# Kernel optimization log

Hardware: AMD Instinct MI355X
Metric: run time of the kernel (lower is better)

The kernel has to match this reference:

```python
import jax, jax.numpy as jnp
import numpy as np
from jax import lax

FIRE_RATE = 0.5
CLIP_ALPHA = 0.1

def _sobel_kernels_3d():
    # (4,1,3,3,3): identity, grad-x, grad-y, grad-z
    g = np.array([1.0, 2.0, 1.0], np.float32)
    s = np.array([1.0, 0.0, -1.0], np.float32)
    sx = np.einsum('i,j,k->ijk', s, g, g) / 16.0
    sy = np.einsum('i,j,k->ijk', g, s, g) / 16.0
    sz = np.einsum('i,j,k->ijk', g, g, s) / 16.0
    ident = np.zeros((3, 3, 3), np.float32)
    ident[1, 1, 1] = 1.0
    return jnp.asarray(np.stack([ident, sx, sy, sz])[:, None])

_KERN = _sobel_kernels_3d()

def _life_mask(state):
    # alive if 3x3x3 max-pooled alpha channel > CLIP_ALPHA
    alpha = state[:, 3:4]
    pooled = lax.reduce_window(alpha, -jnp.inf, lax.max,
                               (1, 1, 3, 3, 3), (1, 1, 1, 1, 1), 'SAME')
    return (pooled > CLIP_ALPHA).astype(state.dtype)

def _perceive(state):
    # depthwise application of the 4 fixed kernels, replicate padding
    n, c, d, h, w = state.shape
    padded = jnp.pad(state, ((0, 0), (0, 0), (1, 1), (1, 1), (1, 1)), mode='edge')
    x = padded.reshape(n * c, 1, d + 2, h + 2, w + 2)
    y = lax.conv_general_dilated(x, _KERN.astype(state.dtype), (1, 1, 1), 'VALID',
                                 dimension_numbers=('NCDHW', 'OIDHW', 'NCDHW'))
    # (n*c,4,d,h,w) -> (n,4,c,d,h,w) -> (n,4c,d,h,w) matches torch concat order
    y = y.reshape(n, c, 4, d, h, w).transpose(0, 2, 1, 3, 4, 5)
    return y.reshape(n, 4 * c, d, h, w)

def setup_inputs() -> dict:
    key = jax.random.key(0)
    k1, k2, k3, k4 = jax.random.split(key, 4)
    N, C, G, H = 4, 16, 64, 96
    state = jax.random.normal(k1, (N, C, G, G, G), dtype=jnp.float32)
    rand_u = jax.random.uniform(k2, (N, 1, G, G, G), dtype=jnp.float32)
    w1 = jax.random.normal(k3, (H, 4 * C), dtype=jnp.float32) * 0.05
    b1 = jnp.zeros((H,), jnp.float32)
    w2 = jax.random.normal(k4, (C, H), dtype=jnp.float32) * 0.05
    return {"state": state, "rand_u": rand_u, "w1": w1, "b1": b1, "w2": w2}

def reference(state, rand_u, w1, b1, w2):
    pre_alive = _life_mask(state)
    perception = _perceive(state)                       # (N,4C,D,H,W)
    hid = jnp.einsum('nxdhw,yx->nydhw', perception, w1) + b1[None, :, None, None, None]
    hid = jax.nn.relu(hid)
    delta = jnp.einsum('nydhw,cy->ncdhw', hid, w2)      # (N,C,D,H,W)
    update_mask = (rand_u < FIRE_RATE).astype(state.dtype)
    new_state = state + delta * update_mask
    post_alive = _life_mask(new_state)
    return new_state * (pre_alive * post_alive)
```

## Files before the change

### kernel.cpp

```cpp
#include <hip/hip_runtime.h>

constexpr int G = 64;
constexpr int C = 16;
constexpr int NBATCH = 4;
constexpr int HID = 96;
constexpr int G3 = G * G * G;

typedef _Float16 h2    __attribute__((ext_vector_type(2)));
typedef _Float16 f16x4 __attribute__((ext_vector_type(4)));
typedef _Float16 f16x8 __attribute__((ext_vector_type(8)));
typedef float    f32x4 __attribute__((ext_vector_type(4)));

__device__ __forceinline__ f32x4 mfma16(f16x8 a, f16x8 b, f32x4 c) {
    return __builtin_amdgcn_mfma_f32_16x16x32_f16(a, b, c, 0, 0, 0);
}

#if __has_builtin(__builtin_amdgcn_global_load_lds)
#define HAS_GLL 1
__device__ __forceinline__ void gload_lds(const float* g, float* l) {
    __builtin_amdgcn_global_load_lds(
        (const __attribute__((address_space(1))) void*)g,
        (__attribute__((address_space(3))) void*)l, 4, 0, 0);
}
#else
#define HAS_GLL 0
#endif

__global__ __launch_bounds__(256)
void nca_packw(const float* __restrict__ w1, const float* __restrict__ w2,
               _Float16* __restrict__ a1p, _Float16* __restrict__ a2p)
{
    const int i = blockIdx.x * 256 + threadIdx.x;
    {
        const int j = i & 7, lane = (i >> 3) & 63, f = i >> 9;
        const int mt = f >> 1, kt = f & 1;
        const int y = mt * 16 + (lane & 15);
        const int x = kt * 32 + ((lane >> 4) << 3) + j;
        a1p[i] = (_Float16)w1[y * 64 + x];
    }
    if (i < 3 * 512) {
        const int j = i & 7, lane = (i >> 3) & 63, kt2 = i >> 9;
        const int c = lane & 15;
        const int y = kt2 * 32 + ((lane >> 4) << 3) + j;
        a2p[i] = (_Float16)w2[c * HID + y];
    }
}

constexpr int HALO_N = 600;
constexpr int BUF_F  = 8 * HALO_N;
constexpr int XROW = 144;
constexpr int HROW = 80;
constexpr int XWAVE = 64 * XROW;

__global__ __launch_bounds__(256, 3)
void nca_update(const float* __restrict__ state, const float* __restrict__ rand_u,
                const _Float16* __restrict__ a1p, const float* __restrict__ b1,
                const _Float16* __restrict__ a2p,
                float* __restrict__ out, float* __restrict__ acopy)
{
    __shared__ __align__(16) char smem[2 * BUF_F * 4];
    float* buf0 = (float*)smem;
    float* buf1 = buf0 + BUF_F;

    const int tid = threadIdx.x;
    const int bid = blockIdx.x;
    const int bx = bid & 7, by = (bid >> 3) & 7, bz = (bid >> 6) & 15, n = bid >> 10;
    const int x0 = bx * 8, y0 = by * 8, z0 = bz * 4;
    const float* sb = state + (size_t)n * C * G3;

    int vo0, vo1, vo2;
    {
        const int j = tid;
        const int lx = j % 10, t = j / 10, ly = t % 10, lz = t / 10;
        vo0 = min(max(z0 + lz - 1, 0), G - 1) * (G * G)
            + min(max(y0 + ly - 1, 0), G - 1) * G
            + min(max(x0 + lx - 1, 0), G - 1);
    }
    {
        const int j = tid + 256;
        const int lx = j % 10, t = j / 10, ly = t % 10, lz = t / 10;
        vo1 = min(max(z0 + lz - 1, 0), G - 1) * (G * G)
            + min(max(y0 + ly - 1, 0), G - 1) * G
            + min(max(x0 + lx - 1, 0), G - 1);
    }
    const bool act2 = (tid + 512 < HALO_N);
    {
        const int j = min(tid + 512, HALO_N - 1);
        const int lx = j % 10, t = j / 10, ly = t % 10, lz = t / 10;
        vo2 = min(max(z0 + lz - 1, 0), G - 1) * (G * G)
            + min(max(y0 + ly - 1, 0), G - 1) * G
            + min(max(x0 + lx - 1, 0), G - 1);
    }
    const int wbase = tid & ~63;

    const int lxl = (tid & 7) + 1, lyl = ((tid >> 3) & 7) + 1, lzl = (tid >> 6) + 1;
    const int cbase = (lzl - 1) * 100 + (lyl - 1) * 10 + (lxl - 1);
    const size_t vofs = (size_t)(z0 + lzl - 1) * (G * G)
                      + (size_t)(y0 + lyl - 1) * G + (x0 + lxl - 1);
    const float ru = rand_u[(size_t)n * G3 + vofs];

#if HAS_GLL
#pragma unroll
    for (int c = 0; c < 8; ++c) {
        const float* gc = sb + (size_t)c * G3;
        gload_lds(gc + vo0, buf0 + c * HALO_N + wbase);
        gload_lds(gc + vo1, buf0 + c * HALO_N + 256 + wbase);
        if (act2) gload_lds(gc + vo2, buf0 + c * HALO_N + 512 + wbase);
    }
    __syncthreads();

#pragma unroll
    for (int c = 0; c < 8; ++c) {
        const float* gc = sb + (size_t)(8 + c) * G3;
        gload_lds(gc + vo0, buf1 + c * HALO_N + wbase);
        gload_lds(gc + vo1, buf1 + c * HALO_N + 256 + wbase);
        if (act2) gload_lds(gc + vo2, buf1 + c * HALO_N + 512 + wbase);
    }
#else
#pragma unroll
    for (int c = 0; c < 8; ++c) {
        const float* gc = sb + (size_t)c * G3;
        buf0[c * HALO_N + tid] = gc[vo0];
        buf0[c * HALO_N + 256 + tid] = gc[vo1];
        if (act2) buf0[c * HALO_N + 512 + tid] = gc[vo2];
    }
    __syncthreads();
#pragma unroll
    for (int c = 0; c < 8; ++c) {
        const float* gc = sb + (size_t)(8 + c) * G3;
        buf1[c * HALO_N + tid] = gc[vo0];
        buf1[c * HALO_N + 256 + tid] = gc[vo1];
        if (act2) buf1[c * HALO_N + 512 + tid] = gc[vo2];
    }
#endif

    h2 pp[32];
    float ctrf[C];
    float pf0 = 0.f, pf1 = 0.f, pf2 = 0.f, pf3 = 0.f;
    float amax = -3.0e38f;

#pragma unroll
    for (int g = 0; g < 2; ++g) {
        const float* bb = g ? buf1 : buf0;
        if (g) __syncthreads();

#pragma unroll
        for (int c = 0; c < 8; ++c) {
            const int cg = g * 8 + c;
            const float* buf = bb + c * HALO_N;
            float P0 = 0.f, P2 = 0.f, U0 = 0.f, U2 = 0.f, V0 = 0.f, V2 = 0.f;
            float ctr = 0.f, mx = -3.0e38f;
#pragma unroll
            for (int dz = 0; dz < 3; ++dz) {
                const float gzw = (dz == 1) ? 2.f : 1.f;
#pragma unroll
                for (int dy = 0; dy < 3; ++dy) {
                    const float gyw = (dy == 1) ? 2.f : 1.f;
                    const float* r = buf + cbase + dz * 100 + dy * 10;
                    const float a0 = r[0], a1 = r[1], a2 = r[2];
                    const float rs = a0 + 2.f * a1 + a2;
                    if (dz == 0) P0 += gyw * rs;
                    if (dz == 2) P2 += gyw * rs;
                    if (dy == 0) U0 += gzw * rs;
                    if (dy == 2) U2 += gzw * rs;
                    V0 += gzw * gyw * a0;
                    V2 += gzw * gyw * a2;
                    if (dz == 1 && dy == 1) ctr = a1;
                    if (cg == 3) mx = fmaxf(mx, fmaxf(fmaxf(a0, a1), a2));
                }
            }
            if (cg == 3) amax = mx;
            ctrf[cg] = ctr;

            const float f0 = ctr;
            const float f1 = (P0 - P2) * 0.0625f;
            const float f2 = (U0 - U2) * 0.0625f;
            const float f3 = (V0 - V2) * 0.0625f;

            if (cg & 1) {
                const int j = cg >> 1;
                h2 v;
                v.x = (_Float16)pf0; v.y = (_Float16)f0; pp[j]      = v;
                v.x = (_Float16)pf1; v.y = (_Float16)f1; pp[8 + j]  = v;
                v.x = (_Float16)pf2; v.y = (_Float16)f2; pp[16 + j] = v;
                v.x = (_Float16)pf3; v.y = (_Float16)f3; pp[24 + j] = v;
            } else {
                pf0 = f0; pf1 = f1; pf2 = f2; pf3 = f3;
            }
        }
    }

    __syncthreads();

    const float pre = (amax > 0.1f) ? 1.f : 0.f;

    const int lane = tid & 63;
    const int w    = tid >> 6;
    const int l15  = lane & 15;
    const int lg   = lane >> 4;
    char* xw = smem + w * XWAVE;

#pragma unroll
    for (int q = 0; q < 8; ++q) {
        uint4 t;
        t.x = __builtin_bit_cast(unsigned, pp[4 * q]);
        t.y = __builtin_bit_cast(unsigned, pp[4 * q + 1]);
        t.z = __builtin_bit_cast(unsigned, pp[4 * q + 2]);
        t.w = __builtin_bit_cast(unsigned, pp[4 * q + 3]);
        *(uint4*)(xw + lane * XROW + q * 16) = t;
    }

    f16x8 bfr[8];
#pragma unroll
    for (int kt = 0; kt < 2; ++kt)
#pragma unroll
        for (int nt = 0; nt < 4; ++nt)
            bfr[kt * 4 + nt] = *(const f16x8*)(xw + (nt * 16 + l15) * XROW + kt * 64 + lg * 16);

    const f16x8* a1 = ((const f16x8*)a1p) + lane;
    const f16x8* a2 = ((const f16x8*)a2p) + lane;

    f32x4 acc2[4];
#pragma unroll
    for (int nt = 0; nt < 4; ++nt) acc2[nt] = (f32x4){0.f, 0.f, 0.f, 0.f};

#pragma unroll 1
    for (int kt2 = 0; kt2 < 3; ++kt2) {
#pragma unroll
        for (int mtsub = 0; mtsub < 2; ++mtsub) {
            const int mt = kt2 * 2 + mtsub;
            const f16x8 a_0 = a1[(mt * 2 + 0) * 64];
            const f16x8 a_1 = a1[(mt * 2 + 1) * 64];
            const f32x4 bias = *(const f32x4*)(b1 + mt * 16 + lg * 4);
#pragma unroll
            for (int nt = 0; nt < 4; ++nt) {
                f32x4 acc = (f32x4){0.f, 0.f, 0.f, 0.f};
                acc = mfma16(a_0, bfr[nt],     acc);
                acc = mfma16(a_1, bfr[4 + nt], acc);
                f16x4 hv;
                hv[0] = (_Float16)fmaxf(acc[0] + bias[0], 0.f);
                hv[1] = (_Float16)fmaxf(acc[1] + bias[1], 0.f);
                hv[2] = (_Float16)fmaxf(acc[2] + bias[2], 0.f);
                hv[3] = (_Float16)fmaxf(acc[3] + bias[3], 0.f);
                *(f16x4*)(xw + (nt * 16 + l15) * HROW + mtsub * 32 + lg * 8) = hv;
            }
        }
        const f16x8 a2f = a2[kt2 * 64];
#pragma unroll
        for (int nt = 0; nt < 4; ++nt) {
            const f16x8 b2 = *(const f16x8*)(xw + (nt * 16 + l15) * HROW + lg * 16);
            acc2[nt] = mfma16(a2f, b2, acc2[nt]);
        }
    }

#pragma unroll
    for (int nt = 0; nt < 4; ++nt) {
        *(f32x4*)(xw + (nt * 16 + l15) * HROW + lg * 16) = acc2[nt];
    }

    const float m = (ru < 0.5f) ? 1.f : 0.f;
    float* ob = out + (size_t)n * C * G3;
    float* ac = acopy + (size_t)n * G3;
#pragma unroll
    for (int q = 0; q < 4; ++q) {
        const f32x4 dv = *(const f32x4*)(xw + lane * HROW + q * 16);
#pragma unroll
        for (int r = 0; r < 4; ++r) {
            const int c = q * 4 + r;
            const float nv = fmaf(dv[r], m, ctrf[c]);
            if (c == 3) ac[vofs] = nv;
            ob[(size_t)c * G3 + vofs] = nv * pre;
        }
    }
}

__global__ __launch_bounds__(256)
void nca_post(const float* __restrict__ acopy, float* __restrict__ out)
{
    const int idx = blockIdx.x * 256 + threadIdx.x;
    const int n = idx >> 18;
    const int v = idx & (G3 - 1);
    const int x = v & 63, y = (v >> 6) & 63, z = v >> 12;
    const float* ab = acopy + (size_t)n * G3;
    float mx = -3.0e38f;
#pragma unroll
    for (int dz = -1; dz <= 1; ++dz) {
        const int zz = min(max(z + dz, 0), G - 1);
#pragma unroll
        for (int dy = -1; dy <= 1; ++dy) {
            const int yy = min(max(y + dy, 0), G - 1);
            const int xm = max(x - 1, 0), xp = min(x + 1, G - 1);
            const float* row = ab + (size_t)zz * (G * G) + (size_t)yy * G;
            mx = fmaxf(mx, fmaxf(fmaxf(row[xm], row[x]), row[xp]));
        }
    }
    if (mx > 0.1f) return;
    float* ob = out + (size_t)n * C * G3 + v;
#pragma unroll
    for (int c = 0; c < C; ++c) ob[(size_t)c * G3] = 0.f;
}

extern "C" void kernel_launch(void* const* d_in, const int* in_sizes, int n_in,
                              void* d_out, int out_size, void* d_ws, size_t ws_size,
                              hipStream_t stream)
{
    const float* state  = (const float*)d_in[0];
    const float* rand_u = (const float*)d_in[1];
    const float* w1     = (const float*)d_in[2];
    const float* b1     = (const float*)d_in[3];
    const float* w2     = (const float*)d_in[4];
    float* out  = (float*)d_out;

    _Float16* a1p  = (_Float16*)d_ws;
    _Float16* a2p  = (_Float16*)((char*)d_ws + 12 * 1024);
    float*    acop = (float*)((char*)d_ws + 16 * 1024);

    nca_packw <<<24, 256, 0, stream>>>(w1, w2, a1p, a2p);
    nca_update<<<NBATCH * 8 * 8 * 16, 256, 0, stream>>>(state, rand_u, a1p, b1, a2p, out, acop);
    nca_post  <<<(NBATCH * G3) / 256, 256, 0, stream>>>(acop, out);
}
```

Measured before the change: 111.4 us.

## Pipeline halo loads in four channel groups and raise occupancy with LDS swizzle

Halo staging now streams four groups of four channels through a ping-pong LDS buffer, so the global-to-LDS loads for the next group overlap the stencil work on the current one. The launch bound rises from 3 to 4 blocks per CU. To cut register use, the per-channel center values are no longer kept in fp32 registers; they are read back from an fp16 side buffer in LDS for the residual add. The MFMA operand tile drops its padding and uses an XOR swizzle to avoid bank conflicts. The trade-offs are more barriers per block and fp16 rounding of the state term in the output, which may affect accuracy.

```diff
diff --git a/kernel.cpp b/kernel.cpp
--- a/kernel.cpp
+++ b/kernel.cpp
@@ -47,20 +47,22 @@
 }
 
 constexpr int HALO_N = 600;
-constexpr int BUF_F  = 8 * HALO_N;
-constexpr int XROW = 144;
-constexpr int HROW = 80;
-constexpr int XWAVE = 64 * XROW;
-
-__global__ __launch_bounds__(256, 3)
+constexpr int GBUF_F = 4 * HALO_N;
+constexpr int XROW   = 128;
+constexpr int XWAVE  = 64 * XROW;
+constexpr int HROW   = 80;
+constexpr int SIDE_OFF = 4 * XWAVE;
+constexpr int SMEM_B = SIDE_OFF + 256 * 32;
+
+__global__ __launch_bounds__(256, 4)
 void nca_update(const float* __restrict__ state, const float* __restrict__ rand_u,
                 const _Float16* __restrict__ a1p, const float* __restrict__ b1,
                 const _Float16* __restrict__ a2p,
                 float* __restrict__ out, float* __restrict__ acopy)
 {
-    __shared__ __align__(16) char smem[2 * BUF_F * 4];
-    float* buf0 = (float*)smem;
-    float* buf1 = buf0 + BUF_F;
+    __shared__ __align__(16) char smem[SMEM_B];
+    float* bufA = (float*)smem;
+    float* bufB = bufA + GBUF_F;
 
     const int tid = threadIdx.x;
     const int bid = blockIdx.x;
@@ -99,54 +101,50 @@
                       + (size_t)(y0 + lyl - 1) * G + (x0 + lxl - 1);
     const float ru = rand_u[(size_t)n * G3 + vofs];
 
-#if HAS_GLL
-#pragma unroll
-    for (int c = 0; c < 8; ++c) {
-        const float* gc = sb + (size_t)c * G3;
-        gload_lds(gc + vo0, buf0 + c * HALO_N + wbase);
-        gload_lds(gc + vo1, buf0 + c * HALO_N + 256 + wbase);
-        if (act2) gload_lds(gc + vo2, buf0 + c * HALO_N + 512 + wbase);
-    }
-    __syncthreads();
-
-#pragma unroll
-    for (int c = 0; c < 8; ++c) {
-        const float* gc = sb + (size_t)(8 + c) * G3;
-        gload_lds(gc + vo0, buf1 + c * HALO_N + wbase);
-        gload_lds(gc + vo1, buf1 + c * HALO_N + 256 + wbase);
-        if (act2) gload_lds(gc + vo2, buf1 + c * HALO_N + 512 + wbase);
-    }
-#else
-#pragma unroll
-    for (int c = 0; c < 8; ++c) {
-        const float* gc = sb + (size_t)c * G3;
-        buf0[c * HALO_N + tid] = gc[vo0];
-        buf0[c * HALO_N + 256 + tid] = gc[vo1];
-        if (act2) buf0[c * HALO_N + 512 + tid] = gc[vo2];
-    }
-    __syncthreads();
-#pragma unroll
-    for (int c = 0; c < 8; ++c) {
-        const float* gc = sb + (size_t)(8 + c) * G3;
-        buf1[c * HALO_N + tid] = gc[vo0];
-        buf1[c * HALO_N + 256 + tid] = gc[vo1];
-        if (act2) buf1[c * HALO_N + 512 + tid] = gc[vo2];
-    }
-#endif
-
     h2 pp[32];
-    float ctrf[C];
     float pf0 = 0.f, pf1 = 0.f, pf2 = 0.f, pf3 = 0.f;
     float amax = -3.0e38f;
 
-#pragma unroll
-    for (int g = 0; g < 2; ++g) {
-        const float* bb = g ? buf1 : buf0;
-        if (g) __syncthreads();
-
-#pragma unroll
-        for (int c = 0; c < 8; ++c) {
-            const int cg = g * 8 + c;
+#if HAS_GLL
+#define STAGE(gi, dst)                                                       \
+    {                                                                        \
+        const float* s4 = sb + (size_t)((gi) * 4) * G3;                      \
+        _Pragma("unroll")                                                    \
+        for (int c = 0; c < 4; ++c) {                                        \
+            const float* gc = s4 + (size_t)c * G3;                           \
+            gload_lds(gc + vo0, (dst) + c * HALO_N + wbase);                 \
+            gload_lds(gc + vo1, (dst) + c * HALO_N + 256 + wbase);           \
+            if (act2) gload_lds(gc + vo2, (dst) + c * HALO_N + 512 + wbase); \
+        }                                                                    \
+    }
+#else
+#define STAGE(gi, dst)                                                       \
+    {                                                                        \
+        const float* s4 = sb + (size_t)((gi) * 4) * G3;                      \
+        _Pragma("unroll")                                                    \
+        for (int c = 0; c < 4; ++c) {                                        \
+            const float* gc = s4 + (size_t)c * G3;                           \
+            (dst)[c * HALO_N + tid] = gc[vo0];                               \
+            (dst)[c * HALO_N + 256 + tid] = gc[vo1];                         \
+            if (act2) (dst)[c * HALO_N + 512 + tid] = gc[vo2];               \
+        }                                                                    \
+    }
+#endif
+
+    STAGE(0, bufA);
+    __syncthreads();
+
+#pragma unroll
+    for (int g = 0; g < 4; ++g) {
+        if (g < 3) {
+            float* nb = (g & 1) ? bufA : bufB;
+            STAGE(g + 1, nb);
+        }
+        const float* bb = (g & 1) ? bufB : bufA;
+
+#pragma unroll
+        for (int c = 0; c < 4; ++c) {
+            const int cg = g * 4 + c;
             const float* buf = bb + c * HALO_N;
             float P0 = 0.f, P2 = 0.f, U0 = 0.f, U2 = 0.f, V0 = 0.f, V2 = 0.f;
             float ctr = 0.f, mx = -3.0e38f;
@@ -170,7 +168,6 @@
                 }
             }
             if (cg == 3) amax = mx;
-            ctrf[cg] = ctr;
 
             const float f0 = ctr;
             const float f1 = (P0 - P2) * 0.0625f;
@@ -188,9 +185,9 @@
                 pf0 = f0; pf1 = f1; pf2 = f2; pf3 = f3;
             }
         }
-    }
-
-    __syncthreads();
+        __syncthreads();
+    }
+#undef STAGE
 
     const float pre = (amax > 0.1f) ? 1.f : 0.f;
 
@@ -198,7 +195,22 @@
     const int w    = tid >> 6;
     const int l15  = lane & 15;
     const int lg   = lane >> 4;
-    char* xw = smem + w * XWAVE;
+    char* xw   = smem + w * XWAVE;
+    char* side = smem + SIDE_OFF + tid * 32;
+
+    {
+        uint4 ia, ib;
+        ia.x = __builtin_bit_cast(unsigned, pp[0]);
+        ia.y = __builtin_bit_cast(unsigned, pp[1]);
+        ia.z = __builtin_bit_cast(unsigned, pp[2]);
+        ia.w = __builtin_bit_cast(unsigned, pp[3]);
+        ib.x = __builtin_bit_cast(unsigned, pp[4]);
+        ib.y = __builtin_bit_cast(unsigned, pp[5]);
+        ib.z = __builtin_bit_cast(unsigned, pp[6]);
+        ib.w = __builtin_bit_cast(unsigned, pp[7]);
+        *(uint4*)(side) = ia;
+        *(uint4*)(side + 16) = ib;
+    }
 
 #pragma unroll
     for (int q = 0; q < 8; ++q) {
@@ -207,15 +219,18 @@
         t.y = __builtin_bit_cast(unsigned, pp[4 * q + 1]);
         t.z = __builtin_bit_cast(unsigned, pp[4 * q + 2]);
         t.w = __builtin_bit_cast(unsigned, pp[4 * q + 3]);
-        *(uint4*)(xw + lane * XROW + q * 16) = t;
+        *(uint4*)(xw + lane * XROW + ((q * 16) ^ ((lane & 7) << 4))) = t;
     }
 
     f16x8 bfr[8];
 #pragma unroll
     for (int kt = 0; kt < 2; ++kt)
 #pragma unroll
-        for (int nt = 0; nt < 4; ++nt)
-            bfr[kt * 4 + nt] = *(const f16x8*)(xw + (nt * 16 + l15) * XROW + kt * 64 + lg * 16);
+        for (int nt = 0; nt < 4; ++nt) {
+            const int v = nt * 16 + l15;
+            bfr[kt * 4 + nt] = *(const f16x8*)(
+                xw + v * XROW + ((kt * 64 + lg * 16) ^ ((v & 7) << 4)));
+        }
 
     const f16x8* a1 = ((const f16x8*)a1p) + lane;
     const f16x8* a2 = ((const f16x8*)a2p) + lane;
@@ -259,6 +274,18 @@
     }
 
     const float m = (ru < 0.5f) ? 1.f : 0.f;
+    const uint4 ia = *(const uint4*)(side);
+    const uint4 ib = *(const uint4*)(side + 16);
+    float s0v[16];
+    {
+        const unsigned wds[8] = {ia.x, ia.y, ia.z, ia.w, ib.x, ib.y, ib.z, ib.w};
+#pragma unroll
+        for (int j = 0; j < 8; ++j) {
+            const h2 p = __builtin_bit_cast(h2, wds[j]);
+            s0v[2 * j]     = (float)p.x;
+            s0v[2 * j + 1] = (float)p.y;
+        }
+    }
     float* ob = out + (size_t)n * C * G3;
     float* ac = acopy + (size_t)n * G3;
 #pragma unroll
@@ -267,7 +294,7 @@
 #pragma unroll
         for (int r = 0; r < 4; ++r) {
             const int c = q * 4 + r;
-            const float nv = fmaf(dv[r], m, ctrf[c]);
+            const float nv = fmaf(dv[r], m, s0v[c]);
             if (c == 3) ac[vofs] = nv;
             ob[(size_t)c * G3 + vofs] = nv * pre;
         }
```

Measured after the change: 241.3 us. +116.6%, slower.
